# Kernel optimization log

Measured on AMD Instinct MI355X. Metric: run time of the kernel, lower is better.

## Reference

```python
import jax, jax.numpy as jnp
import numpy as np

B, F, Q, DIM, H, DH, MULT = 16, 4096, 64, 512, 8, 64, 2
EPS = 1e-5


def _ln(x, g, b):
    m = jnp.mean(x, axis=-1, keepdims=True)
    v = jnp.mean(jnp.square(x - m), axis=-1, keepdims=True)
    return (x - m) * jax.lax.rsqrt(v + EPS) * g + b


def setup_inputs() -> dict:
    key = jax.random.key(0)
    ks = jax.random.split(key, 8)
    s = 0.02
    return {
        "features": jax.random.normal(ks[0], (B, F, DIM), jnp.float32),
        "latents": jax.random.normal(ks[1], (B, Q, DIM), jnp.float32),
        "mask": jax.random.randint(ks[2], (B, F), 0, 2, jnp.int32),
        "gf": jnp.ones((DIM,), jnp.float32),
        "bf": jnp.zeros((DIM,), jnp.float32),
        "gl": jnp.ones((DIM,), jnp.float32),
        "bl": jnp.zeros((DIM,), jnp.float32),
        "Wq": jax.random.normal(ks[3], (DIM, DIM), jnp.float32) * s,
        "Wk": jax.random.normal(ks[4], (DIM, DIM), jnp.float32) * s,
        "Wv": jax.random.normal(ks[5], (DIM, DIM), jnp.float32) * s,
        "gff": jnp.ones((DIM,), jnp.float32),
        "bff": jnp.zeros((DIM,), jnp.float32),
        "W1": jax.random.normal(ks[6], (DIM, MULT * DIM), jnp.float32) * s,
        "W2": jax.random.normal(ks[7], (MULT * DIM, DIM), jnp.float32) * s,
    }


def reference(features, latents, mask, gf, bf, gl, bl, Wq, Wk, Wv, gff, bff, W1, W2):
    scale = DH ** (-0.5)
    x = _ln(features, gf, bf)          # (B, F, DIM)
    lat = _ln(latents, gl, bl)         # (B, Q, DIM)
    q = (lat @ Wq).reshape(B, Q, H, DH).transpose(0, 2, 1, 3)  # b h q d
    k = (x @ Wk).reshape(B, F, H, DH).transpose(0, 2, 1, 3)    # b h f d
    v = (x @ Wv).reshape(B, F, H, DH).transpose(0, 2, 1, 3)    # b h f d
    sim = jnp.einsum('bhqd,bhfd->bhqf', q * scale, k)
    sim = sim - jax.lax.stop_gradient(jnp.max(sim, axis=-1, keepdims=True))
    sim = jnp.where(mask[:, None, None, :] == 0, -jnp.inf, sim)
    alphas = jnp.nan_to_num(jax.nn.softmax(sim, axis=-1), nan=0.0)
    out = jnp.einsum('bhqf,bhfd->bhqd', alphas, v)
    out = out.transpose(0, 2, 1, 3).reshape(B, Q, DIM)         # b q (h d)
    # feed-forward: LN -> Linear -> ReLU -> Linear (no bias)
    h = jax.nn.relu(_ln(out, gff, bff) @ W1)
    return h @ W2
```

## Files before the change

### kernel.cpp

```cpp
#include <hip/hip_runtime.h>
#include <hip/hip_bf16.h>
#include <math.h>

typedef short bf16x8 __attribute__((ext_vector_type(8)));
typedef float f32x4 __attribute__((ext_vector_type(4)));

__device__ __forceinline__ f32x4 mfma16(bf16x8 a, bf16x8 b, f32x4 c) {
    return __builtin_amdgcn_mfma_f32_16x16x32_bf16(a, b, c, 0, 0, 0);
}

__device__ __forceinline__ unsigned short f2b(float f) {
    unsigned int x = __float_as_uint(f);
    unsigned int r = (x + 0x7fffu + ((x >> 16) & 1u)) >> 16;
    return (unsigned short)r;
}

#define GLOBAL_AS(p) ((__attribute__((address_space(1))) void*)(p))
#define LDS_AS(p)    ((__attribute__((address_space(3))) void*)(p))

__global__ __launch_bounds__(256) void prep(const int* __restrict__ mask,
                                            int* __restrict__ cidx,
                                            int* __restrict__ cntp,
                                            const float* __restrict__ Wq,
                                            const float* __restrict__ Wk,
                                            const float* __restrict__ Wv,
                                            const float* __restrict__ W1,
                                            const float* __restrict__ W2,
                                            unsigned short* __restrict__ WqT,
                                            unsigned short* __restrict__ WkT,
                                            unsigned short* __restrict__ WvT,
                                            unsigned short* __restrict__ W1T,
                                            unsigned short* __restrict__ W2T) {
    __shared__ unsigned long long bals[64];
    __shared__ int base[64];
    __shared__ float tile[32][33];
    int bid = blockIdx.x;
    if (bid < 16) {
        int b = bid;
        int tid = threadIdx.x;
        int wave = tid >> 6, lane = tid & 63;
        const int* mb = mask + b * 4096;
#pragma unroll
        for (int k = 0; k < 16; ++k) {
            int g = wave * 16 + k;
            int m = mb[g * 64 + lane] != 0;
            unsigned long long bal = __ballot(m);
            if (lane == 0) bals[g] = bal;
        }
        __syncthreads();
        if (wave == 0) {
            int v = __popcll(bals[lane]);
            int own = v;
#pragma unroll
            for (int off = 1; off < 64; off <<= 1) {
                int n = __shfl_up(v, off);
                if (lane >= off) v += n;
            }
            base[lane] = v - own;
            if (lane == 63) {
                cntp[b] = v;
                cntp[16 + b] = (v + 127) & ~127;
            }
        }
        __syncthreads();
#pragma unroll
        for (int k = 0; k < 16; ++k) {
            int g = wave * 16 + k;
            unsigned long long bal = bals[g];
            int m = (int)((bal >> lane) & 1ull);
            int pre = __popcll(bal & ((1ull << lane) - 1ull));
            if (m) cidx[b * 4096 + base[g] + pre] = g * 64 + lane;
        }
        return;
    }
    int id = bid - 16;
    const float* in; unsigned short* out; int R, C;
    if (id < 256)       { in = Wq; out = WqT; R = 512;  C = 512;  }
    else if (id < 512)  { in = Wk; out = WkT; R = 512;  C = 512;  id -= 256;  }
    else if (id < 768)  { in = Wv; out = WvT; R = 512;  C = 512;  id -= 512;  }
    else if (id < 1280) { in = W1; out = W1T; R = 512;  C = 1024; id -= 768;  }
    else                { in = W2; out = W2T; R = 1024; C = 512;  id -= 1280; }
    int tilesX = C >> 5;
    int c0 = (id % tilesX) * 32, r0 = (id / tilesX) * 32;
    int tx = threadIdx.x & 31, ty = threadIdx.x >> 5;
#pragma unroll
    for (int i = 0; i < 32; i += 8)
        tile[ty + i][tx] = in[(size_t)(r0 + ty + i) * C + c0 + tx];
    __syncthreads();
#pragma unroll
    for (int i = 0; i < 32; i += 8)
        out[(size_t)(c0 + ty + i) * R + r0 + tx] = f2b(tile[tx][ty + i]);
}

__global__ __launch_bounds__(256) void ln_all(const float* __restrict__ feat,
                                              const float* __restrict__ lat,
                                              const int* __restrict__ cidx,
                                              const int* __restrict__ cntp,
                                              const float* __restrict__ gf,
                                              const float* __restrict__ bf_,
                                              const float* __restrict__ gl,
                                              const float* __restrict__ bl,
                                              unsigned short* __restrict__ xn,
                                              unsigned short* __restrict__ latn) {
    int bid = blockIdx.x;
    int lane = threadIdx.x & 63;
    const float* rp; unsigned short* orow; const float *gw, *bw;
    if (bid < 16384) {
        int row = bid * 4 + (threadIdx.x >> 6);
        int b = row >> 12, j = row & 4095;
        int cnt = cntp[b], padded = cntp[16 + b];
        if (j >= padded) return;
        orow = xn + (size_t)row * 512;
        if (j >= cnt) {
            ushort4 z; z.x = z.y = z.z = z.w = 0;
            *(ushort4*)(orow + lane * 4) = z;
            *(ushort4*)(orow + 256 + lane * 4) = z;
            return;
        }
        int src = cidx[b * 4096 + j];
        rp = feat + ((size_t)b * 4096 + src) * 512;
        gw = gf; bw = bf_;
    } else {
        int row = (bid - 16384) * 4 + (threadIdx.x >> 6);
        rp = lat + (size_t)row * 512;
        orow = latn + (size_t)row * 512;
        gw = gl; bw = bl;
    }
    float4 x0 = *(const float4*)(rp + lane * 4);
    float4 x1 = *(const float4*)(rp + 256 + lane * 4);
    float s  = x0.x + x0.y + x0.z + x0.w + x1.x + x1.y + x1.z + x1.w;
    float sq = x0.x*x0.x + x0.y*x0.y + x0.z*x0.z + x0.w*x0.w
             + x1.x*x1.x + x1.y*x1.y + x1.z*x1.z + x1.w*x1.w;
#pragma unroll
    for (int m = 1; m < 64; m <<= 1) {
        s  += __shfl_xor(s, m);
        sq += __shfl_xor(sq, m);
    }
    float mean = s * (1.0f / 512.0f);
    float var  = sq * (1.0f / 512.0f) - mean * mean;
    float rs   = rsqrtf(var + 1e-5f);
    float4 g0 = *(const float4*)(gw + lane * 4);
    float4 g1 = *(const float4*)(gw + 256 + lane * 4);
    float4 b0 = *(const float4*)(bw + lane * 4);
    float4 b1 = *(const float4*)(bw + 256 + lane * 4);
    ushort4 o0, o1;
    o0.x = f2b((x0.x - mean) * rs * g0.x + b0.x);
    o0.y = f2b((x0.y - mean) * rs * g0.y + b0.y);
    o0.z = f2b((x0.z - mean) * rs * g0.z + b0.z);
    o0.w = f2b((x0.w - mean) * rs * g0.w + b0.w);
    o1.x = f2b((x1.x - mean) * rs * g1.x + b1.x);
    o1.y = f2b((x1.y - mean) * rs * g1.y + b1.y);
    o1.z = f2b((x1.z - mean) * rs * g1.z + b1.z);
    o1.w = f2b((x1.w - mean) * rs * g1.w + b1.w);
    *(ushort4*)(orow + lane * 4) = o0;
    *(ushort4*)(orow + 256 + lane * 4) = o1;
}

template <int EPI>
__global__ __launch_bounds__(256) void gemm_bt64(const unsigned short* __restrict__ A,
                                                 const unsigned short* __restrict__ Bt,
                                                 void* __restrict__ Cv,
                                                 int M, int N, int K) {
    __shared__ unsigned short As[2][64 * 32];
    __shared__ unsigned short Bs[2][64 * 32];
    const int tid = threadIdx.x;
    const int wave = tid >> 6, lane = tid & 63;
    const int qd = lane >> 4, cc = lane & 15;
    const int m0 = blockIdx.y * 64, n0 = blockIdx.x * 64;
    const int wm = (wave >> 1) * 32, wn = (wave & 1) * 32;
    const int lrow = wave * 16 + (lane >> 2);
    const int lcol = (lane & 3) * 8;
    f32x4 acc[2][2] = {};

    auto stage = [&](int dst, int kt) {
        const unsigned short* ga = A + (size_t)(m0 + lrow) * K + kt + lcol;
        __builtin_amdgcn_global_load_lds(GLOBAL_AS(ga), LDS_AS(&As[dst][wave * 512]), 16, 0, 0);
        const unsigned short* gb = Bt + (size_t)(n0 + lrow) * K + kt + lcol;
        __builtin_amdgcn_global_load_lds(GLOBAL_AS(gb), LDS_AS(&Bs[dst][wave * 512]), 16, 0, 0);
    };

    int buf = 0;
    stage(0, 0);
    __syncthreads();
    for (int kt = 0; kt < K; kt += 32) {
        if (kt + 32 < K) stage(buf ^ 1, kt + 32);
        bf16x8 af[2], bfr[2];
#pragma unroll
        for (int i = 0; i < 2; ++i)
            af[i] = *(const bf16x8*)&As[buf][(wm + i * 16 + cc) * 32 + qd * 8];
#pragma unroll
        for (int j = 0; j < 2; ++j)
            bfr[j] = *(const bf16x8*)&Bs[buf][(wn + j * 16 + cc) * 32 + qd * 8];
#pragma unroll
        for (int i = 0; i < 2; ++i)
#pragma unroll
            for (int j = 0; j < 2; ++j)
                acc[i][j] = mfma16(af[i], bfr[j], acc[i][j]);
        __syncthreads();
        buf ^= 1;
    }
#pragma unroll
    for (int i = 0; i < 2; ++i) {
#pragma unroll
        for (int j = 0; j < 2; ++j) {
            int row = m0 + wm + i * 16 + qd * 4;
            int col = n0 + wn + j * 16 + cc;
#pragma unroll
            for (int r = 0; r < 4; ++r) {
                float v = acc[i][j][r];
                if (EPI == 1) v = fmaxf(v, 0.0f);
                if (EPI == 2)
                    ((float*)Cv)[(size_t)(row + r) * N + col] = v;
                else
                    ((unsigned short*)Cv)[(size_t)(row + r) * N + col] = f2b(v);
            }
        }
    }
}

__global__ __launch_bounds__(256, 2) void gemm_kv(const unsigned short* __restrict__ Xn,
                                                  const unsigned short* __restrict__ WkT,
                                                  const unsigned short* __restrict__ WvT,
                                                  const int* __restrict__ cntp,
                                                  unsigned short* __restrict__ Kout,
                                                  unsigned short* __restrict__ VTout) {
    const int L = blockIdx.x;
    const int t7 = L >> 3;
    const int c = t7 & 3;
    const int m = ((t7 >> 2) << 3) | (L & 7);
    const int m0 = m * 128;
    const int b = m0 >> 12;
    if ((m0 & 4095) >= cntp[16 + b]) return;
    __shared__ unsigned short Xs[2][128 * 32];
    __shared__ unsigned short Ks[2][128 * 32];
    __shared__ unsigned short Vs[2][128 * 32];
    __shared__ unsigned short stage[128 * 128];
    const int tid = threadIdx.x;
    const int wave = tid >> 6, lane = tid & 63;
    const int qd = lane >> 4, cc = lane & 15;
    const int n0 = c * 128;
    const int wm = (wave >> 1) * 64, wn = (wave & 1) * 64;
    const int lrow = lane >> 2;
    const int lcol = (lane & 3) * 8;
    f32x4 accK[4][4] = {};
    f32x4 accV[4][4] = {};

    auto kvstage = [&](int dst, int kt) {
#pragma unroll
        for (int r = 0; r < 2; ++r) {
            int slab = wave * 16 + r * 64;
            const unsigned short* gx = Xn + (size_t)(m0 + slab + lrow) * 512 + kt + lcol;
            __builtin_amdgcn_global_load_lds(GLOBAL_AS(gx), LDS_AS(&Xs[dst][slab * 32]), 16, 0, 0);
            const unsigned short* gk = WkT + (size_t)(n0 + slab + lrow) * 512 + kt + lcol;
            __builtin_amdgcn_global_load_lds(GLOBAL_AS(gk), LDS_AS(&Ks[dst][slab * 32]), 16, 0, 0);
            const unsigned short* gv = WvT + (size_t)(n0 + slab + lrow) * 512 + kt + lcol;
            __builtin_amdgcn_global_load_lds(GLOBAL_AS(gv), LDS_AS(&Vs[dst][slab * 32]), 16, 0, 0);
        }
    };

    int buf = 0;
    kvstage(0, 0);
    __syncthreads();
    for (int kt = 0; kt < 512; kt += 32) {
        if (kt + 32 < 512) kvstage(buf ^ 1, kt + 32);
        bf16x8 xf[4], kf[4], vf[4];
#pragma unroll
        for (int i = 0; i < 4; ++i)
            xf[i] = *(const bf16x8*)&Xs[buf][(wm + i * 16 + cc) * 32 + qd * 8];
#pragma unroll
        for (int j = 0; j < 4; ++j) {
            kf[j] = *(const bf16x8*)&Ks[buf][(wn + j * 16 + cc) * 32 + qd * 8];
            vf[j] = *(const bf16x8*)&Vs[buf][(wn + j * 16 + cc) * 32 + qd * 8];
        }
#pragma unroll
        for (int i = 0; i < 4; ++i)
#pragma unroll
            for (int j = 0; j < 4; ++j) {
                accK[i][j] = mfma16(xf[i], kf[j], accK[i][j]);
                accV[j][i] = mfma16(vf[j], xf[i], accV[j][i]);
            }
        __syncthreads();
        buf ^= 1;
    }
    const int fbase = m0 & 4095;

#pragma unroll
    for (int i = 0; i < 4; ++i)
#pragma unroll
        for (int j = 0; j < 4; ++j) {
            int row = wm + i * 16 + qd * 4;
            int col = wn + j * 16 + cc;
#pragma unroll
            for (int r = 0; r < 4; ++r)
                stage[(row + r) * 128 + col] = f2b(accK[i][j][r]);
        }
    __syncthreads();
#pragma unroll
    for (int s = 0; s < 2; ++s) {
        int hh = (c << 1) | s;
        char* gbase = (char*)(Kout + ((size_t)(b * 8 + hh) * 4096 + fbase) * 64);
#pragma unroll
        for (int it = 0; it < 4; ++it) {
            int o = it * 4096 + tid * 16;
            int row = o >> 7;
            int inb = o & 127;
            *(bf16x8*)(gbase + o) =
                *(const bf16x8*)((const char*)stage + row * 256 + s * 128 + inb);
        }
    }
    __syncthreads();

#pragma unroll
    for (int j = 0; j < 4; ++j)
#pragma unroll
        for (int i = 0; i < 4; ++i) {
            int d = wn + j * 16 + qd * 4;
            int fl = wm + i * 16 + cc;
#pragma unroll
            for (int r = 0; r < 4; ++r)
                stage[(d + r) * 128 + fl] = f2b(accV[j][i][r]);
        }
    __syncthreads();
#pragma unroll
    for (int hs = 0; hs < 2; ++hs)
#pragma unroll
        for (int ft = 0; ft < 2; ++ft) {
            int hh = (c << 1) | hs;
            int ftile = (fbase >> 6) + ft;
            char* gbase = (char*)(VTout + (size_t)(b * 8 + hh) * 262144
                                        + (size_t)ftile * 4096);
#pragma unroll
            for (int it = 0; it < 2; ++it) {
                int o = it * 4096 + tid * 16;
                int dl = o >> 7;
                int inb = o & 127;
                *(bf16x8*)(gbase + o) =
                    *(const bf16x8*)((const char*)stage + (hs * 64 + dl) * 256
                                     + ft * 128 + inb);
            }
        }
}

__global__ __launch_bounds__(256, 3) void attn_kernel(const unsigned short* __restrict__ Qb,
                                                      const unsigned short* __restrict__ Khm,
                                                      const unsigned short* __restrict__ Vhm,
                                                      const int* __restrict__ cntp,
                                                      float* __restrict__ Opart,
                                                      float* __restrict__ lpart) {
    int blk = blockIdx.x;
    int b = blk >> 5;
    int h = (blk >> 2) & 7;
    int fs = blk & 3;
    int cnt = cntp[b];
    int pad = cntp[16 + b];
    int nchunks = pad >> 6;
    int wave = threadIdx.x >> 6, lane = threadIdx.x & 63;
    int qd = lane >> 4, cc = lane & 15;
    const int qt = wave;

    __shared__ unsigned short Ks[2][64 * 64];
    __shared__ unsigned short Vs[2][64 * 64];
    __shared__ unsigned short p_lds[4][16][72];

    const unsigned short* Kbase = Khm + (size_t)(b * 8 + h) * 262144;
    const unsigned short* Vbase = Vhm + (size_t)(b * 8 + h) * 262144;

    const unsigned short* qrow = Qb + (size_t)(b * 64 + qt * 16 + cc) * 512 + h * 64;
    bf16x8 qf0 = *(const bf16x8*)(qrow + qd * 8);
    bf16x8 qf1 = *(const bf16x8*)(qrow + 32 + qd * 8);
    bf16x8 ones;
#pragma unroll
    for (int j = 0; j < 8; ++j) ones[j] = (short)0x3F80;

    f32x4 O4[4] = {};
    f32x4 lac = {};
    const float cexp = 0.1803368801f;

#define STAGE(dst, cidx) do {                                                       \
        const char* kt_ = (const char*)(Kbase + (size_t)(cidx) * 4096);             \
        const char* vt_ = (const char*)(Vbase + (size_t)(cidx) * 4096);             \
        char* kd_ = (char*)&Ks[dst][0];                                             \
        char* vd_ = (char*)&Vs[dst][0];                                             \
        _Pragma("unroll")                                                           \
        for (int i_ = 0; i_ < 2; ++i_) {                                            \
            int o_ = i_ * 4096 + wave * 1024 + lane * 16;                           \
            int sb_ = o_ ^ (((o_ >> 7) & 7) << 4);                                  \
            __builtin_amdgcn_global_load_lds(GLOBAL_AS(kt_ + sb_),                  \
                LDS_AS(kd_ + i_ * 4096 + wave * 1024), 16, 0, 0);                   \
            __builtin_amdgcn_global_load_lds(GLOBAL_AS(vt_ + sb_),                  \
                LDS_AS(vd_ + i_ * 4096 + wave * 1024), 16, 0, 0);                   \
        }                                                                           \
    } while (0)

    int buf = 0;
    if (fs < nchunks) STAGE(0, fs);
    __syncthreads();

    const int swz = (cc & 7) << 4;
    for (int c = fs; c < nchunks; c += 4) {
        int cn = c + 4;
        if (cn < nchunks) STAGE(buf ^ 1, cn);

        const char* ksb = (const char*)&Ks[buf][0];
        const char* vsb = (const char*)&Vs[buf][0];
        int f0 = c * 64;
        bf16x8 kf[4][2], vf[4][2];
        int mv[4];
#pragma unroll
        for (int t = 0; t < 4; ++t) {
            int rb = (t * 16 + cc) * 128;
            kf[t][0] = *(const bf16x8*)(ksb + rb + ((qd << 4) ^ swz));
            kf[t][1] = *(const bf16x8*)(ksb + rb + ((64 + (qd << 4)) ^ swz));
            mv[t] = (f0 + t * 16 + cc) < cnt;
        }
#pragma unroll
        for (int g = 0; g < 4; ++g) {
            int rb = (g * 16 + cc) * 128;
            vf[g][0] = *(const bf16x8*)(vsb + rb + ((qd << 4) ^ swz));
            vf[g][1] = *(const bf16x8*)(vsb + rb + ((64 + (qd << 4)) ^ swz));
        }
        f32x4 s4[4] = {};
#pragma unroll
        for (int t = 0; t < 4; ++t) {
            s4[t] = mfma16(qf0, kf[t][0], s4[t]);
            s4[t] = mfma16(qf1, kf[t][1], s4[t]);
        }
#pragma unroll
        for (int t = 0; t < 4; ++t)
#pragma unroll
            for (int r = 0; r < 4; ++r) {
                float p = mv[t] ? exp2f(s4[t][r] * cexp) : 0.0f;
                p_lds[wave][qd * 4 + r][t * 16 + cc] = f2b(p);
            }
        bf16x8 pf0 = *(const bf16x8*)&p_lds[wave][cc][qd * 8];
        bf16x8 pf1 = *(const bf16x8*)&p_lds[wave][cc][32 + qd * 8];
        lac = mfma16(pf0, ones, lac);
        lac = mfma16(pf1, ones, lac);
#pragma unroll
        for (int g = 0; g < 4; ++g) {
            O4[g] = mfma16(pf0, vf[g][0], O4[g]);
            O4[g] = mfma16(pf1, vf[g][1], O4[g]);
        }
        __syncthreads();
        buf ^= 1;
    }
#undef STAGE

    float* op = Opart + (size_t)blk * 4096;
#pragma unroll
    for (int g = 0; g < 4; ++g)
#pragma unroll
        for (int r = 0; r < 4; ++r)
            op[(qt * 16 + qd * 4 + r) * 64 + g * 16 + cc] = O4[g][r];
    if (cc == 0) {
#pragma unroll
        for (int r = 0; r < 4; ++r)
            lpart[blk * 64 + qt * 16 + qd * 4 + r] = lac[r];
    }
}

__global__ __launch_bounds__(256) void ln_combine(const float* __restrict__ Opart,
                                                  const float* __restrict__ lpart,
                                                  const float* __restrict__ gw,
                                                  const float* __restrict__ bw,
                                                  unsigned short* __restrict__ out) {
    int row = blockIdx.x * 4 + (threadIdx.x >> 6);
    int lane = threadIdx.x & 63;
    int b = row >> 6, q = row & 63;
    int h = lane >> 3;
    int dh0 = (lane & 7) * 8;
    int blkbase = b * 32 + h * 4;
    float o[8] = {0,0,0,0,0,0,0,0};
    float l = 0.0f;
#pragma unroll
    for (int fsplit = 0; fsplit < 4; ++fsplit) {
        const float* op = Opart + (size_t)(blkbase + fsplit) * 4096 + q * 64 + dh0;
        float4 a0 = *(const float4*)op;
        float4 a1 = *(const float4*)(op + 4);
        o[0] += a0.x; o[1] += a0.y; o[2] += a0.z; o[3] += a0.w;
        o[4] += a1.x; o[5] += a1.y; o[6] += a1.z; o[7] += a1.w;
        l += lpart[(blkbase + fsplit) * 64 + q];
    }
    float inv = (l > 0.0f) ? 1.0f / l : 0.0f;
    float s = 0.0f, sq = 0.0f;
#pragma unroll
    for (int j = 0; j < 8; ++j) { o[j] *= inv; s += o[j]; sq += o[j] * o[j]; }
#pragma unroll
    for (int m = 1; m < 64; m <<= 1) {
        s  += __shfl_xor(s, m);
        sq += __shfl_xor(sq, m);
    }
    float mean = s * (1.0f / 512.0f);
    float var  = sq * (1.0f / 512.0f) - mean * mean;
    float rs   = rsqrtf(var + 1e-5f);
    int d0 = lane * 8;
    float4 g0 = *(const float4*)(gw + d0);
    float4 g1 = *(const float4*)(gw + d0 + 4);
    float4 b0 = *(const float4*)(bw + d0);
    float4 b1 = *(const float4*)(bw + d0 + 4);
    ushort4 w0, w1;
    w0.x = f2b((o[0] - mean) * rs * g0.x + b0.x);
    w0.y = f2b((o[1] - mean) * rs * g0.y + b0.y);
    w0.z = f2b((o[2] - mean) * rs * g0.z + b0.z);
    w0.w = f2b((o[3] - mean) * rs * g0.w + b0.w);
    w1.x = f2b((o[4] - mean) * rs * g1.x + b1.x);
    w1.y = f2b((o[5] - mean) * rs * g1.y + b1.y);
    w1.z = f2b((o[6] - mean) * rs * g1.z + b1.z);
    w1.w = f2b((o[7] - mean) * rs * g1.w + b1.w);
    *(ushort4*)(out + (size_t)row * 512 + d0) = w0;
    *(ushort4*)(out + (size_t)row * 512 + d0 + 4) = w1;
}

extern "C" void kernel_launch(void* const* d_in, const int* in_sizes, int n_in,
                              void* d_out, int out_size, void* d_ws, size_t ws_size,
                              hipStream_t stream) {
    const float* features = (const float*)d_in[0];
    const float* latents  = (const float*)d_in[1];
    const int*   mask     = (const int*)d_in[2];
    const float* gf  = (const float*)d_in[3];
    const float* bf_ = (const float*)d_in[4];
    const float* gl  = (const float*)d_in[5];
    const float* bl  = (const float*)d_in[6];
    const float* Wq  = (const float*)d_in[7];
    const float* Wk  = (const float*)d_in[8];
    const float* Wv  = (const float*)d_in[9];
    const float* gff = (const float*)d_in[10];
    const float* bff = (const float*)d_in[11];
    const float* W1  = (const float*)d_in[12];
    const float* W2  = (const float*)d_in[13];

    char* ws = (char*)d_ws;
    unsigned short* xn   = (unsigned short*)(ws);
    unsigned short* Kbuf = (unsigned short*)(ws + 67108864ull);
    unsigned short* VTb  = (unsigned short*)(ws + 134217728ull);
    unsigned short* latn = (unsigned short*)(ws + 201326592ull);
    unsigned short* Qbuf = (unsigned short*)(ws + 202375168ull);
    unsigned short* ffin = (unsigned short*)(ws + 205520896ull);
    unsigned short* hbuf = (unsigned short*)(ws + 206569472ull);
    unsigned short* WqT  = (unsigned short*)(ws + 208666624ull);
    unsigned short* WkT  = (unsigned short*)(ws + 209190912ull);
    unsigned short* WvT  = (unsigned short*)(ws + 209715200ull);
    unsigned short* W1T  = (unsigned short*)(ws + 210239488ull);
    unsigned short* W2T  = (unsigned short*)(ws + 211288064ull);
    int* cidx = (int*)(ws + 212336640ull);
    int* cntp = (int*)(ws + 212598784ull);
    float* Opart = (float*)(ws);
    float* lpart = (float*)(ws + 8388608ull);

    prep<<<1808, 256, 0, stream>>>(mask, cidx, cntp, Wq, Wk, Wv, W1, W2,
                                   WqT, WkT, WvT, W1T, W2T);

    ln_all<<<16640, 256, 0, stream>>>(features, latents, cidx, cntp,
                                      gf, bf_, gl, bl, xn, latn);

    gemm_kv<<<2048, 256, 0, stream>>>(xn, WkT, WvT, cntp, Kbuf, VTb);
    gemm_bt64<0><<<dim3(8, 16), 256, 0, stream>>>(latn, WqT, Qbuf, 1024, 512, 512);

    attn_kernel<<<512, 256, 0, stream>>>(Qbuf, Kbuf, VTb, cntp, Opart, lpart);
    ln_combine<<<256, 256, 0, stream>>>(Opart, lpart, gff, bff, ffin);

    gemm_bt64<1><<<dim3(16, 16), 256, 0, stream>>>(ffin, W1T, hbuf, 1024, 1024, 512);
    gemm_bt64<2><<<dim3(8, 16), 256, 0, stream>>>(hbuf, W2T, (float*)d_out, 1024, 512, 1024);
}
```

Baseline: 318.5 us.

## Split fused K/V projection GEMM into separate output tiles for higher occupancy

The K/V projection kernel no longer computes K and V tiles together in one block. Each block now computes a single 128-wide output tile over a concatenated [WkT; WvT] weight, which relies on WvT sitting directly after WkT in the workspace. It then writes either the head-major K layout or the transposed V layout. This halves the accumulator registers and cuts LDS use (the stage buffer aliases the input buffers), so launch bounds rise to 3 blocks per CU and the grid doubles. In exchange, each X tile is loaded and staged twice, and correctness depends on the implicit contiguity of the two weight buffers.

```diff
diff --git a/kernel.cpp b/kernel.cpp
--- a/kernel.cpp
+++ b/kernel.cpp
@@ -218,127 +218,121 @@
     }
 }
 
-__global__ __launch_bounds__(256, 2) void gemm_kv(const unsigned short* __restrict__ Xn,
-                                                  const unsigned short* __restrict__ WkT,
-                                                  const unsigned short* __restrict__ WvT,
-                                                  const int* __restrict__ cntp,
-                                                  unsigned short* __restrict__ Kout,
-                                                  unsigned short* __restrict__ VTout) {
+__global__ __launch_bounds__(256, 3) void gemm_kvu(const unsigned short* __restrict__ Xn,
+                                                   const unsigned short* __restrict__ WT,
+                                                   const int* __restrict__ cntp,
+                                                   unsigned short* __restrict__ Kout,
+                                                   unsigned short* __restrict__ VTout) {
     const int L = blockIdx.x;
-    const int t7 = L >> 3;
-    const int c = t7 & 3;
-    const int m = ((t7 >> 2) << 3) | (L & 7);
+    const int nt = (L >> 3) & 7;
+    const int m = ((L >> 6) << 3) | (L & 7);
     const int m0 = m * 128;
     const int b = m0 >> 12;
     if ((m0 & 4095) >= cntp[16 + b]) return;
-    __shared__ unsigned short Xs[2][128 * 32];
-    __shared__ unsigned short Ks[2][128 * 32];
-    __shared__ unsigned short Vs[2][128 * 32];
-    __shared__ unsigned short stage[128 * 128];
+    __shared__ unsigned short smem[16384];
+    unsigned short* Xs = smem;
+    unsigned short* Ws = smem + 8192;
+    unsigned short* stage = smem;
     const int tid = threadIdx.x;
     const int wave = tid >> 6, lane = tid & 63;
     const int qd = lane >> 4, cc = lane & 15;
-    const int n0 = c * 128;
+    const int n0 = nt * 128;
     const int wm = (wave >> 1) * 64, wn = (wave & 1) * 64;
     const int lrow = lane >> 2;
     const int lcol = (lane & 3) * 8;
-    f32x4 accK[4][4] = {};
-    f32x4 accV[4][4] = {};
-
-    auto kvstage = [&](int dst, int kt) {
+    f32x4 acc[4][4] = {};
+
+    auto stg = [&](int dst, int kt) {
 #pragma unroll
         for (int r = 0; r < 2; ++r) {
             int slab = wave * 16 + r * 64;
             const unsigned short* gx = Xn + (size_t)(m0 + slab + lrow) * 512 + kt + lcol;
-            __builtin_amdgcn_global_load_lds(GLOBAL_AS(gx), LDS_AS(&Xs[dst][slab * 32]), 16, 0, 0);
-            const unsigned short* gk = WkT + (size_t)(n0 + slab + lrow) * 512 + kt + lcol;
-            __builtin_amdgcn_global_load_lds(GLOBAL_AS(gk), LDS_AS(&Ks[dst][slab * 32]), 16, 0, 0);
-            const unsigned short* gv = WvT + (size_t)(n0 + slab + lrow) * 512 + kt + lcol;
-            __builtin_amdgcn_global_load_lds(GLOBAL_AS(gv), LDS_AS(&Vs[dst][slab * 32]), 16, 0, 0);
+            __builtin_amdgcn_global_load_lds(GLOBAL_AS(gx), LDS_AS(&Xs[dst * 4096 + slab * 32]), 16, 0, 0);
+            const unsigned short* gw = WT + (size_t)(n0 + slab + lrow) * 512 + kt + lcol;
+            __builtin_amdgcn_global_load_lds(GLOBAL_AS(gw), LDS_AS(&Ws[dst * 4096 + slab * 32]), 16, 0, 0);
         }
     };
 
     int buf = 0;
-    kvstage(0, 0);
+    stg(0, 0);
     __syncthreads();
     for (int kt = 0; kt < 512; kt += 32) {
-        if (kt + 32 < 512) kvstage(buf ^ 1, kt + 32);
-        bf16x8 xf[4], kf[4], vf[4];
+        if (kt + 32 < 512) stg(buf ^ 1, kt + 32);
+        bf16x8 xf[4], wf[4];
 #pragma unroll
         for (int i = 0; i < 4; ++i)
-            xf[i] = *(const bf16x8*)&Xs[buf][(wm + i * 16 + cc) * 32 + qd * 8];
-#pragma unroll
-        for (int j = 0; j < 4; ++j) {
-            kf[j] = *(const bf16x8*)&Ks[buf][(wn + j * 16 + cc) * 32 + qd * 8];
-            vf[j] = *(const bf16x8*)&Vs[buf][(wn + j * 16 + cc) * 32 + qd * 8];
-        }
+            xf[i] = *(const bf16x8*)&Xs[buf * 4096 + (wm + i * 16 + cc) * 32 + qd * 8];
+#pragma unroll
+        for (int j = 0; j < 4; ++j)
+            wf[j] = *(const bf16x8*)&Ws[buf * 4096 + (wn + j * 16 + cc) * 32 + qd * 8];
 #pragma unroll
         for (int i = 0; i < 4; ++i)
 #pragma unroll
+            for (int j = 0; j < 4; ++j)
+                acc[i][j] = mfma16(xf[i], wf[j], acc[i][j]);
+        __syncthreads();
+        buf ^= 1;
+    }
+    const int fbase = m0 & 4095;
+
+    if (nt < 4) {
+#pragma unroll
+        for (int i = 0; i < 4; ++i)
+#pragma unroll
             for (int j = 0; j < 4; ++j) {
-                accK[i][j] = mfma16(xf[i], kf[j], accK[i][j]);
-                accV[j][i] = mfma16(vf[j], xf[i], accV[j][i]);
-            }
-        __syncthreads();
-        buf ^= 1;
-    }
-    const int fbase = m0 & 4095;
-
-#pragma unroll
-    for (int i = 0; i < 4; ++i)
-#pragma unroll
-        for (int j = 0; j < 4; ++j) {
-            int row = wm + i * 16 + qd * 4;
-            int col = wn + j * 16 + cc;
-#pragma unroll
-            for (int r = 0; r < 4; ++r)
-                stage[(row + r) * 128 + col] = f2b(accK[i][j][r]);
-        }
-    __syncthreads();
-#pragma unroll
-    for (int s = 0; s < 2; ++s) {
-        int hh = (c << 1) | s;
-        char* gbase = (char*)(Kout + ((size_t)(b * 8 + hh) * 4096 + fbase) * 64);
-#pragma unroll
-        for (int it = 0; it < 4; ++it) {
-            int o = it * 4096 + tid * 16;
-            int row = o >> 7;
-            int inb = o & 127;
-            *(bf16x8*)(gbase + o) =
-                *(const bf16x8*)((const char*)stage + row * 256 + s * 128 + inb);
-        }
-    }
-    __syncthreads();
-
-#pragma unroll
-    for (int j = 0; j < 4; ++j)
-#pragma unroll
-        for (int i = 0; i < 4; ++i) {
-            int d = wn + j * 16 + qd * 4;
-            int fl = wm + i * 16 + cc;
-#pragma unroll
-            for (int r = 0; r < 4; ++r)
-                stage[(d + r) * 128 + fl] = f2b(accV[j][i][r]);
-        }
-    __syncthreads();
-#pragma unroll
-    for (int hs = 0; hs < 2; ++hs)
-#pragma unroll
-        for (int ft = 0; ft < 2; ++ft) {
-            int hh = (c << 1) | hs;
-            int ftile = (fbase >> 6) + ft;
-            char* gbase = (char*)(VTout + (size_t)(b * 8 + hh) * 262144
-                                        + (size_t)ftile * 4096);
-#pragma unroll
-            for (int it = 0; it < 2; ++it) {
+                int row = wm + i * 16 + qd * 4;
+                int col = wn + j * 16 + cc;
+#pragma unroll
+                for (int r = 0; r < 4; ++r)
+                    stage[(row + r) * 128 + col] = f2b(acc[i][j][r]);
+            }
+        __syncthreads();
+#pragma unroll
+        for (int s = 0; s < 2; ++s) {
+            int hh = (nt << 1) | s;
+            char* gbase = (char*)(Kout + ((size_t)(b * 8 + hh) * 4096 + fbase) * 64);
+#pragma unroll
+            for (int it = 0; it < 4; ++it) {
                 int o = it * 4096 + tid * 16;
-                int dl = o >> 7;
+                int row = o >> 7;
                 int inb = o & 127;
                 *(bf16x8*)(gbase + o) =
-                    *(const bf16x8*)((const char*)stage + (hs * 64 + dl) * 256
-                                     + ft * 128 + inb);
-            }
-        }
+                    *(const bf16x8*)((const char*)stage + row * 256 + s * 128 + inb);
+            }
+        }
+    } else {
+        const int cv = nt - 4;
+#pragma unroll
+        for (int i = 0; i < 4; ++i)
+#pragma unroll
+            for (int j = 0; j < 4; ++j) {
+                int d  = wn + j * 16 + cc;
+                int f0 = wm + i * 16 + qd * 4;
+                ushort4 w;
+                w.x = f2b(acc[i][j][0]); w.y = f2b(acc[i][j][1]);
+                w.z = f2b(acc[i][j][2]); w.w = f2b(acc[i][j][3]);
+                *(ushort4*)&stage[d * 128 + f0] = w;
+            }
+        __syncthreads();
+#pragma unroll
+        for (int hs = 0; hs < 2; ++hs)
+#pragma unroll
+            for (int ft = 0; ft < 2; ++ft) {
+                int hh = (cv << 1) | hs;
+                int ftile = (fbase >> 6) + ft;
+                char* gbase = (char*)(VTout + (size_t)(b * 8 + hh) * 262144
+                                            + (size_t)ftile * 4096);
+#pragma unroll
+                for (int it = 0; it < 2; ++it) {
+                    int o = it * 4096 + tid * 16;
+                    int dl = o >> 7;
+                    int inb = o & 127;
+                    *(bf16x8*)(gbase + o) =
+                        *(const bf16x8*)((const char*)stage + (hs * 64 + dl) * 256
+                                         + ft * 128 + inb);
+                }
+            }
+    }
 }
 
 __global__ __launch_bounds__(256, 3) void attn_kernel(const unsigned short* __restrict__ Qb,
@@ -553,7 +547,7 @@
     ln_all<<<16640, 256, 0, stream>>>(features, latents, cidx, cntp,
                                       gf, bf_, gl, bl, xn, latn);
 
-    gemm_kv<<<2048, 256, 0, stream>>>(xn, WkT, WvT, cntp, Kbuf, VTb);
+    gemm_kvu<<<4096, 256, 0, stream>>>(xn, WkT, cntp, Kbuf, VTb);
     gemm_bt64<0><<<dim3(8, 16), 256, 0, stream>>>(latn, WqT, Qbuf, 1024, 512, 512);
 
     attn_kernel<<<512, 256, 0, stream>>>(Qbuf, Kbuf, VTb, cntp, Opart, lpart);
```

After: 325.8 us. 2.3% more time.
